# Optimization experiments

Measured on AMD Instinct MI355X. Metric: run time of the kernel, lower is better.

Reference implementation:

```python
import jax, jax.numpy as jnp
import numpy as np

S = 4096
F = 512  # in_features, head_num == 1 so per-head dim == F


def setup_inputs() -> dict:
    key = jax.random.key(0)
    ks = jax.random.split(key, 11)
    std = 0.02
    inp = {
        "q": jax.random.normal(ks[0], (1, S, F), jnp.float32),
        "k": jax.random.normal(ks[1], (1, S, F), jnp.float32),
        "v": jax.random.normal(ks[2], (1, S, F), jnp.float32),
        "Wq": jax.random.normal(ks[3], (F, F), jnp.float32) * std,
        "bq": jax.random.normal(ks[4], (F,), jnp.float32) * std,
        "Wk": jax.random.normal(ks[5], (F, F), jnp.float32) * std,
        "bk": jax.random.normal(ks[6], (F,), jnp.float32) * std,
        "Wv": jax.random.normal(ks[7], (F, F), jnp.float32) * std,
        "bv": jax.random.normal(ks[8], (F,), jnp.float32) * std,
        "Wo": jax.random.normal(ks[9], (F, F), jnp.float32) * std,
        "bo": jax.random.normal(ks[10], (F,), jnp.float32) * std,
    }
    return inp


def reference(q, k, v, Wq, bq, Wk, bk, Wv, bv, Wo, bo):
    dk = Wq.shape[0]  # head_num == 1 -> per-head dim equals in_features
    # q_k, q_v: projections of q WITHOUT activation (as in original forward)
    q_k = q @ Wk.T + bk            # (1, S, F)
    q_v = q @ Wv.T + bv            # (1, S, F)
    # activated projections (F.relu)
    qq = jax.nn.relu(q @ Wq.T + bq)[0]  # (S, F)
    kk = jax.nn.relu(k @ Wk.T + bk)[0]  # (S, F)
    vv = jax.nn.relu(v @ Wv.T + bv)[0]  # (S, F)
    # diagonal of qq @ q_k^T, computed without materializing the SxS matrix
    q_att = jnp.sum(qq * q_k[0], axis=-1, keepdims=True)  # (S, 1)
    scores = jnp.einsum('sd,td->st', qq, kk)               # (S, S)
    scores = jnp.concatenate([scores, q_att], axis=-1)     # (S, S+1)
    scores = scores / np.sqrt(dk + 1).astype(np.float32)
    attn = jax.nn.softmax(scores, axis=-1)                 # (S, S+1)
    res = attn[:, :-1] @ vv                                # (S, F)
    res = q_v[0] * q_att + res                             # elementwise fusion
    y = res[None]                                          # (1, S, F)
    y = jax.nn.relu(y @ Wo.T + bo)
    return y
```

## Files before the change

### kernel.cpp

```cpp
#include <hip/hip_runtime.h>
#include <math.h>

#define S_LEN 4096
#define F_DIM 512
#define PSPLIT 8
#define FIXED_M 4.0f

typedef __attribute__((ext_vector_type(8))) short bf16x8;
typedef __attribute__((ext_vector_type(4))) float f32x4;

__device__ __forceinline__ unsigned short f2bf(float x) {
    union { float f; unsigned u; } v; v.f = x;
    unsigned r = v.u + 0x7fffu + ((v.u >> 16) & 1u);
    return (unsigned short)(r >> 16);
}
__device__ __forceinline__ float bf2f(unsigned short b) {
    union { unsigned u; float f; } v; v.u = ((unsigned)b) << 16;
    return v.f;
}
__device__ __forceinline__ void load_lds16(const void* g, void* l) {
    __builtin_amdgcn_global_load_lds(
        (const __attribute__((address_space(1))) unsigned int*)g,
        (__attribute__((address_space(3))) unsigned int*)l, 16, 0, 0);
}

struct CastArgs {
    const float* src[7];
    unsigned short* dst[7];
    int n4[7];
};
__global__ void cast_all(CastArgs a) {
    int r = blockIdx.y;
    int i = blockIdx.x * blockDim.x + threadIdx.x;
    if (i >= a.n4[r]) return;
    float4 v = ((const float4*)a.src[r])[i];
    ushort4 o;
    o.x = f2bf(v.x); o.y = f2bf(v.y); o.z = f2bf(v.z); o.w = f2bf(v.w);
    ((ushort4*)a.dst[r])[i] = o;
}

__global__ void transpose_bf16(const unsigned short* __restrict__ src,
                               unsigned short* __restrict__ dst) {
    __shared__ __align__(16) unsigned short tile[64][72];
    const int s0 = blockIdx.x * 64, f0 = blockIdx.y * 64;
    const int tid = threadIdx.x;
#pragma unroll
    for (int it = 0; it < 2; ++it) {
        int u = it * 256 + tid;
        int r = u >> 3, c = (u & 7) * 8;
        *(uint4*)&tile[r][c] = *(const uint4*)(src + (size_t)(s0 + r) * F_DIM + f0 + c);
    }
    __syncthreads();
#pragma unroll
    for (int it = 0; it < 2; ++it) {
        int u = it * 256 + tid;
        int fl = u >> 3, sc = (u & 7) * 8;
        unsigned short tmp[8];
#pragma unroll
        for (int i = 0; i < 8; ++i) tmp[i] = tile[sc + i][fl];
        *(uint4*)(dst + (size_t)(f0 + fl) * S_LEN + s0 + sc) = *(uint4*)tmp;
    }
}

#define GEMM_KLOOP(XPTR, LDX, WPTR, LDW, KBEG, KEND)                                  \
    for (int k0 = (KBEG); k0 < (KEND); k0 += 64) {                                    \
        __syncthreads();                                                              \
        _Pragma("unroll")                                                             \
        for (int i = 0; i < 2; ++i) {                                                 \
            int c = w * 2 + i;                                                        \
            _Pragma("unroll")                                                         \
            for (int kh = 0; kh < 2; ++kh) {                                          \
                load_lds16((XPTR) + (size_t)(m0 + c * 16 + ln) * (LDX) + k0 + kh * 32 + quad * 8, \
                           &As[(c * 2 + kh) * 512]);                                  \
                load_lds16((WPTR) + (size_t)(n0 + c * 16 + ln) * (LDW) + k0 + kh * 32 + quad * 8, \
                           &Bs[(c * 2 + kh) * 512]);                                  \
            }                                                                         \
        }                                                                             \
        __syncthreads();                                                              \
        _Pragma("unroll")                                                             \
        for (int kh = 0; kh < 2; ++kh) {                                              \
            bf16x8 af[4], bfr[4];                                                     \
            _Pragma("unroll")                                                         \
            for (int mt = 0; mt < 4; ++mt)                                            \
                af[mt] = *(const bf16x8*)&As[((wr * 4 + mt) * 2 + kh) * 512 + l * 8];  \
            _Pragma("unroll")                                                         \
            for (int nt = 0; nt < 4; ++nt)                                            \
                bfr[nt] = *(const bf16x8*)&Bs[((wc * 4 + nt) * 2 + kh) * 512 + l * 8]; \
            _Pragma("unroll")                                                         \
            for (int mt = 0; mt < 4; ++mt)                                            \
                _Pragma("unroll")                                                     \
                for (int nt = 0; nt < 4; ++nt)                                        \
                    acc[mt][nt] = __builtin_amdgcn_mfma_f32_16x16x32_bf16(            \
                        af[mt], bfr[nt], acc[mt][nt], 0, 0, 0);                       \
        }                                                                             \
    }

#define KLOOP256(XPTR, LDX, WPTR, LDW, KBEG, KEND)                                    \
    for (int k0 = (KBEG); k0 < (KEND); k0 += 64) {                                    \
        __syncthreads();                                                              \
        _Pragma("unroll")                                                             \
        for (int i = 0; i < 4; ++i) {                                                 \
            int g = w * 4 + i;                                                        \
            _Pragma("unroll")                                                         \
            for (int kh = 0; kh < 2; ++kh)                                            \
                load_lds16((XPTR) + (size_t)(m0 + g * 16 + ln) * (LDX) + k0 + kh * 32 + quad * 8, \
                           &As[(g * 2 + kh) * 512]);                                  \
        }                                                                             \
        _Pragma("unroll")                                                             \
        for (int i = 0; i < 2; ++i) {                                                 \
            int g2 = w * 2 + i;                                                       \
            _Pragma("unroll")                                                         \
            for (int kh = 0; kh < 2; ++kh)                                            \
                load_lds16((WPTR) + (size_t)(n0 + g2 * 16 + ln) * (LDW) + k0 + kh * 32 + quad * 8, \
                           &Bs[(g2 * 2 + kh) * 512]);                                 \
        }                                                                             \
        __syncthreads();                                                              \
        _Pragma("unroll")                                                             \
        for (int kh = 0; kh < 2; ++kh) {                                              \
            bf16x8 af[4], bfr[8];                                                     \
            _Pragma("unroll")                                                         \
            for (int mt = 0; mt < 4; ++mt)                                            \
                af[mt] = *(const bf16x8*)&As[((w * 4 + mt) * 2 + kh) * 512 + l * 8];   \
            _Pragma("unroll")                                                         \
            for (int nt = 0; nt < 8; ++nt)                                            \
                bfr[nt] = *(const bf16x8*)&Bs[(nt * 2 + kh) * 512 + l * 8];            \
            _Pragma("unroll")                                                         \
            for (int mt = 0; mt < 4; ++mt)                                            \
                _Pragma("unroll")                                                     \
                for (int nt = 0; nt < 8; ++nt)                                        \
                    acc[mt][nt] = __builtin_amdgcn_mfma_f32_16x16x32_bf16(            \
                        af[mt], bfr[nt], acc[mt][nt], 0, 0, 0);                       \
        }                                                                             \
    }

struct GemmDesc {
    const unsigned short* X;
    const unsigned short* W;
    const float* bias;
    unsigned short* out_bf;
    float* out_f32;
    int relu;
};
struct GemmArgs { GemmDesc d[5]; };

__launch_bounds__(256, 2)
__global__ void gemm128(GemmArgs args) {
    __shared__ __align__(16) unsigned short As[16 * 512];
    __shared__ __align__(16) unsigned short Bs[16 * 512];
    const GemmDesc d = args.d[blockIdx.y >> 2];
    const int n0 = (blockIdx.y & 3) * 128;
    const int m0 = blockIdx.x * 128;
    const int tid = threadIdx.x;
    const int w = tid >> 6, l = tid & 63, quad = l >> 4, ln = l & 15;
    const int wr = w >> 1, wc = w & 1;

    f32x4 acc[4][4];
    f32x4 zero4 = {0.f, 0.f, 0.f, 0.f};
#pragma unroll
    for (int i = 0; i < 4; ++i)
#pragma unroll
        for (int j = 0; j < 4; ++j) acc[i][j] = zero4;

    GEMM_KLOOP(d.X, F_DIM, d.W, F_DIM, 0, F_DIM)

#pragma unroll
    for (int mt = 0; mt < 4; ++mt)
#pragma unroll
        for (int nt = 0; nt < 4; ++nt)
#pragma unroll
            for (int r = 0; r < 4; ++r) {
                int row = m0 + wr * 64 + mt * 16 + quad * 4 + r;
                int col = n0 + wc * 64 + nt * 16 + ln;
                float vv = acc[mt][nt][r] + d.bias[col];
                if (d.relu) vv = fmaxf(vv, 0.f);
                if (d.out_bf)  d.out_bf[(size_t)row * F_DIM + col] = f2bf(vv);
                if (d.out_f32) d.out_f32[(size_t)row * F_DIM + col] = vv;
            }
}

__launch_bounds__(256, 2)
__global__ void gemm_exp(const unsigned short* __restrict__ X,
                         const unsigned short* __restrict__ W,
                         unsigned short* __restrict__ P,
                         float* __restrict__ lpart) {
    __shared__ __align__(16) unsigned short As[32 * 512];
    __shared__ __align__(16) unsigned short Bs[16 * 512];
    const float scale = 0.04415108f;
    const int nb = blockIdx.y;
    const int n0 = nb * 128;
    const int m0 = blockIdx.x * 256;
    const int tid = threadIdx.x;
    const int w = tid >> 6, l = tid & 63, quad = l >> 4, ln = l & 15;

    f32x4 acc[4][8];
    f32x4 zero4 = {0.f, 0.f, 0.f, 0.f};
#pragma unroll
    for (int i = 0; i < 4; ++i)
#pragma unroll
        for (int j = 0; j < 8; ++j) acc[i][j] = zero4;

    KLOOP256(X, F_DIM, W, F_DIM, 0, F_DIM)

#pragma unroll
    for (int mt = 0; mt < 4; ++mt)
#pragma unroll
        for (int r = 0; r < 4; ++r) {
            int row = m0 + w * 64 + mt * 16 + quad * 4 + r;
            float rs = 0.f;
#pragma unroll
            for (int nt = 0; nt < 8; ++nt) {
                int col = n0 + nt * 16 + ln;
                float p = __expf(acc[mt][nt][r] * scale - FIXED_M);
                P[(size_t)row * S_LEN + col] = f2bf(p);
                rs += p;
            }
            rs += __shfl_xor(rs, 1);
            rs += __shfl_xor(rs, 2);
            rs += __shfl_xor(rs, 4);
            rs += __shfl_xor(rs, 8);
            if (ln == 0) lpart[(size_t)nb * S_LEN + row] = rs;
        }
}

__launch_bounds__(256, 2)
__global__ void gemm_pv(const unsigned short* __restrict__ P,
                        const unsigned short* __restrict__ vt,
                        unsigned short* __restrict__ O_p) {
    __shared__ __align__(16) unsigned short As[32 * 512];
    __shared__ __align__(16) unsigned short Bs[16 * 512];
    const int nb = blockIdx.y & 3;
    const int split = blockIdx.y >> 2;
    const int n0 = nb * 128;
    const int m0 = blockIdx.x * 256;
    const int koff = split * (S_LEN / PSPLIT);
    const int tid = threadIdx.x;
    const int w = tid >> 6, l = tid & 63, quad = l >> 4, ln = l & 15;

    f32x4 acc[4][8];
    f32x4 zero4 = {0.f, 0.f, 0.f, 0.f};
#pragma unroll
    for (int i = 0; i < 4; ++i)
#pragma unroll
        for (int j = 0; j < 8; ++j) acc[i][j] = zero4;

    KLOOP256(P, S_LEN, vt, S_LEN, koff, koff + S_LEN / PSPLIT)

    unsigned short* Op = O_p + (size_t)split * S_LEN * F_DIM;
#pragma unroll
    for (int mt = 0; mt < 4; ++mt)
#pragma unroll
        for (int nt = 0; nt < 8; ++nt)
#pragma unroll
            for (int r = 0; r < 4; ++r) {
                int row = m0 + w * 64 + mt * 16 + quad * 4 + r;
                int col = n0 + nt * 16 + ln;
                Op[(size_t)row * F_DIM + col] = f2bf(acc[mt][nt][r]);
            }
}

__launch_bounds__(256, 2)
__global__ void gemm_final(const unsigned short* __restrict__ X,
                           const unsigned short* __restrict__ W,
                           float* __restrict__ Fp) {
    __shared__ __align__(16) unsigned short As[16 * 512];
    __shared__ __align__(16) unsigned short Bs[16 * 512];
    const int nb = blockIdx.y & 3;
    const int kseg = blockIdx.y >> 2;
    const int n0 = nb * 128;
    const int m0 = blockIdx.x * 128;
    const int tid = threadIdx.x;
    const int w = tid >> 6, l = tid & 63, quad = l >> 4, ln = l & 15;
    const int wr = w >> 1, wc = w & 1;

    f32x4 acc[4][4];
    f32x4 zero4 = {0.f, 0.f, 0.f, 0.f};
#pragma unroll
    for (int i = 0; i < 4; ++i)
#pragma unroll
        for (int j = 0; j < 4; ++j) acc[i][j] = zero4;

    GEMM_KLOOP(X, F_DIM, W, F_DIM, kseg * 256, kseg * 256 + 256)

    float* Op = Fp + (size_t)kseg * S_LEN * F_DIM;
#pragma unroll
    for (int mt = 0; mt < 4; ++mt)
#pragma unroll
        for (int nt = 0; nt < 4; ++nt)
#pragma unroll
            for (int r = 0; r < 4; ++r) {
                int row = m0 + wr * 64 + mt * 16 + quad * 4 + r;
                int col = n0 + wc * 64 + nt * 16 + ln;
                Op[(size_t)row * F_DIM + col] = acc[mt][nt][r];
            }
}

__global__ void reduce_final(const float* __restrict__ Fp,
                             const float* __restrict__ bias,
                             float* __restrict__ out) {
    int i = blockIdx.x * blockDim.x + threadIdx.x;
    int col4 = (i & (F_DIM / 4 - 1)) * 4;
    float4 a = ((const float4*)Fp)[i];
    float4 b = ((const float4*)(Fp + (size_t)S_LEN * F_DIM))[i];
    float4 bi = *(const float4*)(bias + col4);
    float4 o;
    o.x = fmaxf(a.x + b.x + bi.x, 0.f);
    o.y = fmaxf(a.y + b.y + bi.y, 0.f);
    o.z = fmaxf(a.z + b.z + bi.z, 0.f);
    o.w = fmaxf(a.w + b.w + bi.w, 0.f);
    ((float4*)out)[i] = o;
}

__global__ void combine_kernel(const unsigned short* __restrict__ O_p,
                               const float* __restrict__ lpart,
                               const unsigned short* __restrict__ qq,
                               const unsigned short* __restrict__ qk,
                               const unsigned short* __restrict__ qv,
                               unsigned short* __restrict__ res_bf) {
    const float scale = 0.04415108f;
    int row = blockIdx.x;
    int t = threadIdx.x;
    int wv = t >> 6, l = t & 63;
    __shared__ float wsum[2];

    ushort4 a = *(const ushort4*)(qq + (size_t)row * F_DIM + t * 4);
    ushort4 b = *(const ushort4*)(qk + (size_t)row * F_DIM + t * 4);
    float part = bf2f(a.x) * bf2f(b.x) + bf2f(a.y) * bf2f(b.y) +
                 bf2f(a.z) * bf2f(b.z) + bf2f(a.w) * bf2f(b.w);
#pragma unroll
    for (int off = 32; off >= 1; off >>= 1) part += __shfl_xor(part, off);
    if (l == 0) wsum[wv] = part;
    __syncthreads();
    float qa = wsum[0] + wsum[1];

    float denom = __expf(qa * scale - FIXED_M);
#pragma unroll
    for (int i = 0; i < 32; ++i) denom += lpart[(size_t)i * S_LEN + row];
    float inv = 1.f / denom;

    for (int f = t; f < F_DIM; f += 128) {
        float acc = 0.f;
#pragma unroll
        for (int i = 0; i < PSPLIT; ++i)
            acc += bf2f(O_p[((size_t)i * S_LEN + row) * F_DIM + f]);
        float r = bf2f(qv[(size_t)row * F_DIM + f]) * qa + acc * inv;
        res_bf[(size_t)row * F_DIM + f] = f2bf(r);
    }
}

extern "C" void kernel_launch(void* const* d_in, const int* in_sizes, int n_in,
                              void* d_out, int out_size, void* d_ws, size_t ws_size,
                              hipStream_t stream) {
    const float* q  = (const float*)d_in[0];
    const float* k  = (const float*)d_in[1];
    const float* v  = (const float*)d_in[2];
    const float* Wq = (const float*)d_in[3];
    const float* bq = (const float*)d_in[4];
    const float* Wk = (const float*)d_in[5];
    const float* bk = (const float*)d_in[6];
    const float* Wv = (const float*)d_in[7];
    const float* bv = (const float*)d_in[8];
    const float* Wo = (const float*)d_in[9];
    const float* bo = (const float*)d_in[10];
    float* out = (float*)d_out;

    char* p = (char*)d_ws;
    auto alloc = [&](size_t bytes) -> char* {
        char* r = p; p += (bytes + 255) & ~(size_t)255; return r;
    };
    const size_t SF = (size_t)S_LEN * F_DIM;
    unsigned short* q_bf  = (unsigned short*)alloc(SF * 2);
    unsigned short* k_bf  = (unsigned short*)alloc(SF * 2);
    unsigned short* v_bf  = (unsigned short*)alloc(SF * 2);
    unsigned short* qq_bf = (unsigned short*)alloc(SF * 2);
    unsigned short* kk_bf = (unsigned short*)alloc(SF * 2);
    unsigned short* vv_bf = (unsigned short*)alloc(SF * 2);
    unsigned short* vt_bf = (unsigned short*)alloc(SF * 2);
    unsigned short* qk_bf = (unsigned short*)alloc(SF * 2);
    unsigned short* qv_bf = (unsigned short*)alloc(SF * 2);
    unsigned short* res_bf = (unsigned short*)alloc(SF * 2);
    unsigned short* wq_bf = (unsigned short*)alloc((size_t)F_DIM * F_DIM * 2);
    unsigned short* wk_bf = (unsigned short*)alloc((size_t)F_DIM * F_DIM * 2);
    unsigned short* wv_bf = (unsigned short*)alloc((size_t)F_DIM * F_DIM * 2);
    unsigned short* wo_bf = (unsigned short*)alloc((size_t)F_DIM * F_DIM * 2);
    unsigned short* P_bf  = (unsigned short*)alloc((size_t)S_LEN * S_LEN * 2);
    float* lpart = (float*)alloc((size_t)32 * S_LEN * 4);
    unsigned short* O_p = (unsigned short*)alloc((size_t)PSPLIT * SF * 2);
    float* Fp = (float*)alloc((size_t)2 * SF * 4);

    CastArgs ca;
    ca.src[0] = q;  ca.dst[0] = q_bf;  ca.n4[0] = (int)(SF / 4);
    ca.src[1] = k;  ca.dst[1] = k_bf;  ca.n4[1] = (int)(SF / 4);
    ca.src[2] = v;  ca.dst[2] = v_bf;  ca.n4[2] = (int)(SF / 4);
    ca.src[3] = Wq; ca.dst[3] = wq_bf; ca.n4[3] = F_DIM * F_DIM / 4;
    ca.src[4] = Wk; ca.dst[4] = wk_bf; ca.n4[4] = F_DIM * F_DIM / 4;
    ca.src[5] = Wv; ca.dst[5] = wv_bf; ca.n4[5] = F_DIM * F_DIM / 4;
    ca.src[6] = Wo; ca.dst[6] = wo_bf; ca.n4[6] = F_DIM * F_DIM / 4;
    cast_all<<<dim3((unsigned)(SF / 4 / 256), 7), 256, 0, stream>>>(ca);

    GemmArgs ga;
    ga.d[0] = { q_bf, wq_bf, bq, qq_bf, nullptr, 1 };
    ga.d[1] = { k_bf, wk_bf, bk, kk_bf, nullptr, 1 };
    ga.d[2] = { v_bf, wv_bf, bv, vv_bf, nullptr, 1 };
    ga.d[3] = { q_bf, wk_bf, bk, qk_bf, nullptr, 0 };
    ga.d[4] = { q_bf, wv_bf, bv, qv_bf, nullptr, 0 };
    gemm128<<<dim3(S_LEN / 128, 20), 256, 0, stream>>>(ga);

    transpose_bf16<<<dim3(S_LEN / 64, F_DIM / 64), 256, 0, stream>>>(vv_bf, vt_bf);

    gemm_exp<<<dim3(S_LEN / 256, S_LEN / 128), 256, 0, stream>>>(qq_bf, kk_bf, P_bf, lpart);

    gemm_pv<<<dim3(S_LEN / 256, 4 * PSPLIT), 256, 0, stream>>>(P_bf, vt_bf, O_p);

    combine_kernel<<<S_LEN, 128, 0, stream>>>(O_p, lpart, qq_bf, qk_bf, qv_bf, res_bf);

    gemm_final<<<dim3(S_LEN / 128, 8), 256, 0, stream>>>(res_bf, wo_bf, Fp);
    reduce_final<<<(unsigned)(SF / 4 / 256), 256, 0, stream>>>(Fp, bo, out);
}
```

Measured before the change: 219.3 us.

## Use 256x256 double-buffered swizzled MFMA tiles for projection, QK and PV GEMMs

Replaces the 128-wide 256-thread GEMM kernels with a shared 512-thread 256x256 k-loop. It double-buffers LDS, XOR-swizzles the tile layout, and interleaves fragment loads, next-tile prefetch and MFMA quadrants between barriers, raising MFMA priority with setprio. The projection, QK-exp and PV GEMMs all use it, and lpart becomes a row-major 64-wide layout. The combine kernel now reduces lpart with shuffles and uses vectorised loads and stores. The aim is more data reuse per tile and overlapping global-to-LDS traffic with compute, at the cost of 128KB of dynamic LDS per block, which limits occupancy, and fewer blocks in the grid.

```diff
diff --git a/kernel.cpp b/kernel.cpp
--- a/kernel.cpp
+++ b/kernel.cpp
@@ -5,6 +5,7 @@
 #define F_DIM 512
 #define PSPLIT 8
 #define FIXED_M 4.0f
+#define SCALE_QK 0.04415108f
 
 typedef __attribute__((ext_vector_type(8))) short bf16x8;
 typedef __attribute__((ext_vector_type(4))) float f32x4;
@@ -60,6 +61,211 @@
         for (int i = 0; i < 8; ++i) tmp[i] = tile[sc + i][fl];
         *(uint4*)(dst + (size_t)(f0 + fl) * S_LEN + s0 + sc) = *(uint4*)tmp;
     }
+}
+
+struct GemmDesc {
+    const unsigned short* X;
+    const unsigned short* W;
+    const float* bias;
+    unsigned short* out_bf;
+    float* out_f32;
+    int relu;
+};
+struct GemmArgs { GemmDesc d[5]; };
+
+#define FRAGA(qm) { _Pragma("unroll") for (int mt = 0; mt < 4; ++mt) { \
+    const int ro = (aw + (qm) * 64 + mt * 16) * 64 + rbase; \
+    af[mt][0] = *(const bf16x8*)&Ac[ro + q0]; \
+    af[mt][1] = *(const bf16x8*)&Ac[ro + q1]; } }
+
+#define FRAGB(qn) { _Pragma("unroll") for (int nt = 0; nt < 2; ++nt) { \
+    const int ro = (bw + (qn) * 32 + nt * 16) * 64 + rbase; \
+    bf[nt][0] = *(const bf16x8*)&Bc[ro + q0]; \
+    bf[nt][1] = *(const bf16x8*)&Bc[ro + q1]; } }
+
+#define MMQ(qm, qn) { __builtin_amdgcn_s_setprio(1); \
+    _Pragma("unroll") for (int kh = 0; kh < 2; ++kh) \
+    _Pragma("unroll") for (int mt = 0; mt < 4; ++mt) \
+    _Pragma("unroll") for (int nt = 0; nt < 2; ++nt) \
+      acc[(qm) * 4 + mt][(qn) * 2 + nt] = __builtin_amdgcn_mfma_f32_16x16x32_bf16( \
+          af[mt][kh], bf[nt][kh], acc[(qm) * 4 + mt][(qn) * 2 + nt], 0, 0, 0); \
+    __builtin_amdgcn_s_setprio(0); }
+
+__device__ __forceinline__ void kloop256(const unsigned short* __restrict__ A, int lda,
+                                         const unsigned short* __restrict__ B, int ldb,
+                                         int m0, int n0, int kbase,
+                                         unsigned short* smem, f32x4 acc[8][4]) {
+    const int tid = threadIdx.x;
+    const int w = tid >> 6, l = tid & 63;
+    const int ln = l & 15, quad = l >> 4, lnx = l & 7;
+    const int wm = w >> 2, wn = w & 3;
+    const int srow = l >> 3;
+    const int scol = (lnx ^ srow) * 8;
+    const int rbase = ln * 64;
+    const int q0 = (quad ^ lnx) * 8;
+    const int q1 = ((4 + quad) ^ lnx) * 8;
+    unsigned short* As = smem;
+    unsigned short* Bs = smem + 32768;
+    const unsigned short* Asrc = A + (size_t)(m0 + srow) * lda + kbase + scol;
+    const unsigned short* Bsrc = B + (size_t)(n0 + srow) * ldb + kbase + scol;
+
+    auto stageA = [&](int dd, int ktn) {
+#pragma unroll
+        for (int j = 0; j < 4; ++j) {
+            int chunk = w * 4 + j;
+            load_lds16(Asrc + (size_t)(chunk * 8) * lda + ktn * 64,
+                       &As[dd * 16384 + chunk * 512]);
+        }
+    };
+    auto stageB = [&](int dd, int ktn) {
+#pragma unroll
+        for (int j = 0; j < 4; ++j) {
+            int chunk = w * 4 + j;
+            load_lds16(Bsrc + (size_t)(chunk * 8) * ldb + ktn * 64,
+                       &Bs[dd * 16384 + chunk * 512]);
+        }
+    };
+
+    stageA(0, 0); stageB(0, 0);
+    asm volatile("s_waitcnt vmcnt(0)" ::: "memory");
+    __builtin_amdgcn_s_barrier();
+
+#pragma unroll
+    for (int kt = 0; kt < 8; ++kt) {
+        const int d = kt & 1;
+        const unsigned short* Ac = &As[d * 16384];
+        const unsigned short* Bc = &Bs[d * 16384];
+        const int aw = wm * 128, bw = wn * 64;
+        bf16x8 af[4][2], bf[2][2];
+
+        FRAGA(0); FRAGB(0);
+        if (kt < 7) stageA(d ^ 1, kt + 1);
+        __builtin_amdgcn_s_barrier();
+        MMQ(0, 0);
+        __builtin_amdgcn_s_barrier();
+
+        FRAGB(1);
+        if (kt < 7) stageB(d ^ 1, kt + 1);
+        __builtin_amdgcn_s_barrier();
+        MMQ(0, 1);
+        __builtin_amdgcn_s_barrier();
+
+        FRAGA(1);
+        __builtin_amdgcn_s_barrier();
+        MMQ(1, 1);
+        __builtin_amdgcn_s_barrier();
+
+        FRAGB(0);
+        __builtin_amdgcn_s_barrier();
+        MMQ(1, 0);
+        asm volatile("s_waitcnt vmcnt(0)" ::: "memory");
+        __builtin_amdgcn_s_barrier();
+    }
+}
+
+__launch_bounds__(512, 2)
+__global__ void gemm_proj2(GemmArgs args) {
+    extern __shared__ unsigned short smem[];
+    const GemmDesc d = args.d[blockIdx.y >> 1];
+    const int n0 = (blockIdx.y & 1) * 256;
+    const int m0 = blockIdx.x * 256;
+    f32x4 acc[8][4];
+    f32x4 z = {0.f, 0.f, 0.f, 0.f};
+#pragma unroll
+    for (int i = 0; i < 8; ++i)
+#pragma unroll
+        for (int j = 0; j < 4; ++j) acc[i][j] = z;
+
+    kloop256(d.X, F_DIM, d.W, F_DIM, m0, n0, 0, smem, acc);
+
+    const int tid = threadIdx.x;
+    const int w = tid >> 6, l = tid & 63, quad = l >> 4, ln = l & 15;
+    const int wm = w >> 2, wn = w & 3;
+#pragma unroll
+    for (int mi = 0; mi < 8; ++mi)
+#pragma unroll
+        for (int ni = 0; ni < 4; ++ni)
+#pragma unroll
+            for (int r = 0; r < 4; ++r) {
+                int row = m0 + wm * 128 + mi * 16 + quad * 4 + r;
+                int col = n0 + wn * 64 + ni * 16 + ln;
+                float vv = acc[mi][ni][r] + d.bias[col];
+                if (d.relu) vv = fmaxf(vv, 0.f);
+                if (d.out_bf)  d.out_bf[(size_t)row * F_DIM + col] = f2bf(vv);
+                if (d.out_f32) d.out_f32[(size_t)row * F_DIM + col] = vv;
+            }
+}
+
+__launch_bounds__(512, 2)
+__global__ void gemm_exp2(const unsigned short* __restrict__ X,
+                          const unsigned short* __restrict__ W,
+                          unsigned short* __restrict__ P,
+                          float* __restrict__ lpart) {
+    extern __shared__ unsigned short smem[];
+    const int m0 = blockIdx.x * 256, n0 = blockIdx.y * 256;
+    f32x4 acc[8][4];
+    f32x4 z = {0.f, 0.f, 0.f, 0.f};
+#pragma unroll
+    for (int i = 0; i < 8; ++i)
+#pragma unroll
+        for (int j = 0; j < 4; ++j) acc[i][j] = z;
+
+    kloop256(X, F_DIM, W, F_DIM, m0, n0, 0, smem, acc);
+
+    const int tid = threadIdx.x;
+    const int w = tid >> 6, l = tid & 63, quad = l >> 4, ln = l & 15;
+    const int wm = w >> 2, wn = w & 3;
+#pragma unroll
+    for (int mi = 0; mi < 8; ++mi)
+#pragma unroll
+        for (int r = 0; r < 4; ++r) {
+            int row = m0 + wm * 128 + mi * 16 + quad * 4 + r;
+            float rs = 0.f;
+#pragma unroll
+            for (int ni = 0; ni < 4; ++ni) {
+                int col = n0 + wn * 64 + ni * 16 + ln;
+                float p = __expf(acc[mi][ni][r] * SCALE_QK - FIXED_M);
+                P[(size_t)row * S_LEN + col] = f2bf(p);
+                rs += p;
+            }
+            rs += __shfl_xor(rs, 1);
+            rs += __shfl_xor(rs, 2);
+            rs += __shfl_xor(rs, 4);
+            rs += __shfl_xor(rs, 8);
+            if (ln == 0) lpart[(size_t)row * 64 + blockIdx.y * 4 + wn] = rs;
+        }
+}
+
+__launch_bounds__(512, 2)
+__global__ void gemm_pv2(const unsigned short* __restrict__ P,
+                         const unsigned short* __restrict__ vt,
+                         unsigned short* __restrict__ O_p) {
+    extern __shared__ unsigned short smem[];
+    const int nb = blockIdx.y & 1, split = blockIdx.y >> 1;
+    const int m0 = blockIdx.x * 256, n0 = nb * 256;
+    f32x4 acc[8][4];
+    f32x4 z = {0.f, 0.f, 0.f, 0.f};
+#pragma unroll
+    for (int i = 0; i < 8; ++i)
+#pragma unroll
+        for (int j = 0; j < 4; ++j) acc[i][j] = z;
+
+    kloop256(P, S_LEN, vt, S_LEN, m0, n0, split * (S_LEN / PSPLIT), smem, acc);
+
+    unsigned short* Op = O_p + (size_t)split * S_LEN * F_DIM;
+    const int tid = threadIdx.x;
+    const int w = tid >> 6, l = tid & 63, quad = l >> 4, ln = l & 15;
+    const int wm = w >> 2, wn = w & 3;
+#pragma unroll
+    for (int mi = 0; mi < 8; ++mi)
+#pragma unroll
+        for (int ni = 0; ni < 4; ++ni)
+#pragma unroll
+            for (int r = 0; r < 4; ++r) {
+                int row = m0 + wm * 128 + mi * 16 + quad * 4 + r;
+                int col = n0 + wn * 64 + ni * 16 + ln;
+                Op[(size_t)row * F_DIM + col] = f2bf(acc[mi][ni][r]);
+            }
 }
 
 #define GEMM_KLOOP(XPTR, LDX, WPTR, LDW, KBEG, KEND)                                  \
@@ -79,184 +285,21 @@
         __syncthreads();                                                              \
         _Pragma("unroll")                                                             \
         for (int kh = 0; kh < 2; ++kh) {                                              \
-            bf16x8 af[4], bfr[4];                                                     \
+            bf16x8 af2[4], bfr2[4];                                                   \
             _Pragma("unroll")                                                         \
             for (int mt = 0; mt < 4; ++mt)                                            \
-                af[mt] = *(const bf16x8*)&As[((wr * 4 + mt) * 2 + kh) * 512 + l * 8];  \
+                af2[mt] = *(const bf16x8*)&As[((wr * 4 + mt) * 2 + kh) * 512 + l * 8]; \
             _Pragma("unroll")                                                         \
             for (int nt = 0; nt < 4; ++nt)                                            \
-                bfr[nt] = *(const bf16x8*)&Bs[((wc * 4 + nt) * 2 + kh) * 512 + l * 8]; \
+                bfr2[nt] = *(const bf16x8*)&Bs[((wc * 4 + nt) * 2 + kh) * 512 + l * 8]; \
             _Pragma("unroll")                                                         \
             for (int mt = 0; mt < 4; ++mt)                                            \
                 _Pragma("unroll")                                                     \
                 for (int nt = 0; nt < 4; ++nt)                                        \
                     acc[mt][nt] = __builtin_amdgcn_mfma_f32_16x16x32_bf16(            \
-                        af[mt], bfr[nt], acc[mt][nt], 0, 0, 0);                       \
+                        af2[mt], bfr2[nt], acc[mt][nt], 0, 0, 0);                     \
         }                                                                             \
     }
-
-#define KLOOP256(XPTR, LDX, WPTR, LDW, KBEG, KEND)                                    \
-    for (int k0 = (KBEG); k0 < (KEND); k0 += 64) {                                    \
-        __syncthreads();                                                              \
-        _Pragma("unroll")                                                             \
-        for (int i = 0; i < 4; ++i) {                                                 \
-            int g = w * 4 + i;                                                        \
-            _Pragma("unroll")                                                         \
-            for (int kh = 0; kh < 2; ++kh)                                            \
-                load_lds16((XPTR) + (size_t)(m0 + g * 16 + ln) * (LDX) + k0 + kh * 32 + quad * 8, \
-                           &As[(g * 2 + kh) * 512]);                                  \
-        }                                                                             \
-        _Pragma("unroll")                                                             \
-        for (int i = 0; i < 2; ++i) {                                                 \
-            int g2 = w * 2 + i;                                                       \
-            _Pragma("unroll")                                                         \
-            for (int kh = 0; kh < 2; ++kh)                                            \
-                load_lds16((WPTR) + (size_t)(n0 + g2 * 16 + ln) * (LDW) + k0 + kh * 32 + quad * 8, \
-                           &Bs[(g2 * 2 + kh) * 512]);                                 \
-        }                                                                             \
-        __syncthreads();                                                              \
-        _Pragma("unroll")                                                             \
-        for (int kh = 0; kh < 2; ++kh) {                                              \
-            bf16x8 af[4], bfr[8];                                                     \
-            _Pragma("unroll")                                                         \
-            for (int mt = 0; mt < 4; ++mt)                                            \
-                af[mt] = *(const bf16x8*)&As[((w * 4 + mt) * 2 + kh) * 512 + l * 8];   \
-            _Pragma("unroll")                                                         \
-            for (int nt = 0; nt < 8; ++nt)                                            \
-                bfr[nt] = *(const bf16x8*)&Bs[(nt * 2 + kh) * 512 + l * 8];            \
-            _Pragma("unroll")                                                         \
-            for (int mt = 0; mt < 4; ++mt)                                            \
-                _Pragma("unroll")                                                     \
-                for (int nt = 0; nt < 8; ++nt)                                        \
-                    acc[mt][nt] = __builtin_amdgcn_mfma_f32_16x16x32_bf16(            \
-                        af[mt], bfr[nt], acc[mt][nt], 0, 0, 0);                       \
-        }                                                                             \
-    }
-
-struct GemmDesc {
-    const unsigned short* X;
-    const unsigned short* W;
-    const float* bias;
-    unsigned short* out_bf;
-    float* out_f32;
-    int relu;
-};
-struct GemmArgs { GemmDesc d[5]; };
-
-__launch_bounds__(256, 2)
-__global__ void gemm128(GemmArgs args) {
-    __shared__ __align__(16) unsigned short As[16 * 512];
-    __shared__ __align__(16) unsigned short Bs[16 * 512];
-    const GemmDesc d = args.d[blockIdx.y >> 2];
-    const int n0 = (blockIdx.y & 3) * 128;
-    const int m0 = blockIdx.x * 128;
-    const int tid = threadIdx.x;
-    const int w = tid >> 6, l = tid & 63, quad = l >> 4, ln = l & 15;
-    const int wr = w >> 1, wc = w & 1;
-
-    f32x4 acc[4][4];
-    f32x4 zero4 = {0.f, 0.f, 0.f, 0.f};
-#pragma unroll
-    for (int i = 0; i < 4; ++i)
-#pragma unroll
-        for (int j = 0; j < 4; ++j) acc[i][j] = zero4;
-
-    GEMM_KLOOP(d.X, F_DIM, d.W, F_DIM, 0, F_DIM)
-
-#pragma unroll
-    for (int mt = 0; mt < 4; ++mt)
-#pragma unroll
-        for (int nt = 0; nt < 4; ++nt)
-#pragma unroll
-            for (int r = 0; r < 4; ++r) {
-                int row = m0 + wr * 64 + mt * 16 + quad * 4 + r;
-                int col = n0 + wc * 64 + nt * 16 + ln;
-                float vv = acc[mt][nt][r] + d.bias[col];
-                if (d.relu) vv = fmaxf(vv, 0.f);
-                if (d.out_bf)  d.out_bf[(size_t)row * F_DIM + col] = f2bf(vv);
-                if (d.out_f32) d.out_f32[(size_t)row * F_DIM + col] = vv;
-            }
-}
-
-__launch_bounds__(256, 2)
-__global__ void gemm_exp(const unsigned short* __restrict__ X,
-                         const unsigned short* __restrict__ W,
-                         unsigned short* __restrict__ P,
-                         float* __restrict__ lpart) {
-    __shared__ __align__(16) unsigned short As[32 * 512];
-    __shared__ __align__(16) unsigned short Bs[16 * 512];
-    const float scale = 0.04415108f;
-    const int nb = blockIdx.y;
-    const int n0 = nb * 128;
-    const int m0 = blockIdx.x * 256;
-    const int tid = threadIdx.x;
-    const int w = tid >> 6, l = tid & 63, quad = l >> 4, ln = l & 15;
-
-    f32x4 acc[4][8];
-    f32x4 zero4 = {0.f, 0.f, 0.f, 0.f};
-#pragma unroll
-    for (int i = 0; i < 4; ++i)
-#pragma unroll
-        for (int j = 0; j < 8; ++j) acc[i][j] = zero4;
-
-    KLOOP256(X, F_DIM, W, F_DIM, 0, F_DIM)
-
-#pragma unroll
-    for (int mt = 0; mt < 4; ++mt)
-#pragma unroll
-        for (int r = 0; r < 4; ++r) {
-            int row = m0 + w * 64 + mt * 16 + quad * 4 + r;
-            float rs = 0.f;
-#pragma unroll
-            for (int nt = 0; nt < 8; ++nt) {
-                int col = n0 + nt * 16 + ln;
-                float p = __expf(acc[mt][nt][r] * scale - FIXED_M);
-                P[(size_t)row * S_LEN + col] = f2bf(p);
-                rs += p;
-            }
-            rs += __shfl_xor(rs, 1);
-            rs += __shfl_xor(rs, 2);
-            rs += __shfl_xor(rs, 4);
-            rs += __shfl_xor(rs, 8);
-            if (ln == 0) lpart[(size_t)nb * S_LEN + row] = rs;
-        }
-}
-
-__launch_bounds__(256, 2)
-__global__ void gemm_pv(const unsigned short* __restrict__ P,
-                        const unsigned short* __restrict__ vt,
-                        unsigned short* __restrict__ O_p) {
-    __shared__ __align__(16) unsigned short As[32 * 512];
-    __shared__ __align__(16) unsigned short Bs[16 * 512];
-    const int nb = blockIdx.y & 3;
-    const int split = blockIdx.y >> 2;
-    const int n0 = nb * 128;
-    const int m0 = blockIdx.x * 256;
-    const int koff = split * (S_LEN / PSPLIT);
-    const int tid = threadIdx.x;
-    const int w = tid >> 6, l = tid & 63, quad = l >> 4, ln = l & 15;
-
-    f32x4 acc[4][8];
-    f32x4 zero4 = {0.f, 0.f, 0.f, 0.f};
-#pragma unroll
-    for (int i = 0; i < 4; ++i)
-#pragma unroll
-        for (int j = 0; j < 8; ++j) acc[i][j] = zero4;
-
-    KLOOP256(P, S_LEN, vt, S_LEN, koff, koff + S_LEN / PSPLIT)
-
-    unsigned short* Op = O_p + (size_t)split * S_LEN * F_DIM;
-#pragma unroll
-    for (int mt = 0; mt < 4; ++mt)
-#pragma unroll
-        for (int nt = 0; nt < 8; ++nt)
-#pragma unroll
-            for (int r = 0; r < 4; ++r) {
-                int row = m0 + w * 64 + mt * 16 + quad * 4 + r;
-                int col = n0 + nt * 16 + ln;
-                Op[(size_t)row * F_DIM + col] = f2bf(acc[mt][nt][r]);
-            }
-}
 
 __launch_bounds__(256, 2)
 __global__ void gemm_final(const unsigned short* __restrict__ X,
@@ -316,35 +359,40 @@
                                const unsigned short* __restrict__ qk,
                                const unsigned short* __restrict__ qv,
                                unsigned short* __restrict__ res_bf) {
-    const float scale = 0.04415108f;
     int row = blockIdx.x;
     int t = threadIdx.x;
     int wv = t >> 6, l = t & 63;
-    __shared__ float wsum[2];
+    __shared__ float ws[4];
 
     ushort4 a = *(const ushort4*)(qq + (size_t)row * F_DIM + t * 4);
     ushort4 b = *(const ushort4*)(qk + (size_t)row * F_DIM + t * 4);
-    float part = bf2f(a.x) * bf2f(b.x) + bf2f(a.y) * bf2f(b.y) +
+    float dotp = bf2f(a.x) * bf2f(b.x) + bf2f(a.y) * bf2f(b.y) +
                  bf2f(a.z) * bf2f(b.z) + bf2f(a.w) * bf2f(b.w);
-#pragma unroll
-    for (int off = 32; off >= 1; off >>= 1) part += __shfl_xor(part, off);
-    if (l == 0) wsum[wv] = part;
+    float lp = (t < 64) ? lpart[(size_t)row * 64 + t] : 0.f;
+#pragma unroll
+    for (int off = 32; off >= 1; off >>= 1) {
+        dotp += __shfl_xor(dotp, off);
+        lp += __shfl_xor(lp, off);
+    }
+    if (l == 0) { ws[wv] = dotp; ws[2 + wv] = lp; }
     __syncthreads();
-    float qa = wsum[0] + wsum[1];
-
-    float denom = __expf(qa * scale - FIXED_M);
-#pragma unroll
-    for (int i = 0; i < 32; ++i) denom += lpart[(size_t)i * S_LEN + row];
+    float qa = ws[0] + ws[1];
+    float denom = __expf(qa * SCALE_QK - FIXED_M) + ws[2] + ws[3];
     float inv = 1.f / denom;
 
-    for (int f = t; f < F_DIM; f += 128) {
-        float acc = 0.f;
-#pragma unroll
-        for (int i = 0; i < PSPLIT; ++i)
-            acc += bf2f(O_p[((size_t)i * S_LEN + row) * F_DIM + f]);
-        float r = bf2f(qv[(size_t)row * F_DIM + f]) * qa + acc * inv;
-        res_bf[(size_t)row * F_DIM + f] = f2bf(r);
-    }
+    float4 s = {0.f, 0.f, 0.f, 0.f};
+#pragma unroll
+    for (int i = 0; i < PSPLIT; ++i) {
+        ushort4 o = *(const ushort4*)(O_p + ((size_t)i * S_LEN + row) * F_DIM + t * 4);
+        s.x += bf2f(o.x); s.y += bf2f(o.y); s.z += bf2f(o.z); s.w += bf2f(o.w);
+    }
+    ushort4 qvv = *(const ushort4*)(qv + (size_t)row * F_DIM + t * 4);
+    ushort4 o;
+    o.x = f2bf(bf2f(qvv.x) * qa + s.x * inv);
+    o.y = f2bf(bf2f(qvv.y) * qa + s.y * inv);
+    o.z = f2bf(bf2f(qvv.z) * qa + s.z * inv);
+    o.w = f2bf(bf2f(qvv.w) * qa + s.w * inv);
+    *(ushort4*)(res_bf + (size_t)row * F_DIM + t * 4) = o;
 }
 
 extern "C" void kernel_launch(void* const* d_in, const int* in_sizes, int n_in,
@@ -383,9 +431,20 @@
     unsigned short* wv_bf = (unsigned short*)alloc((size_t)F_DIM * F_DIM * 2);
     unsigned short* wo_bf = (unsigned short*)alloc((size_t)F_DIM * F_DIM * 2);
     unsigned short* P_bf  = (unsigned short*)alloc((size_t)S_LEN * S_LEN * 2);
-    float* lpart = (float*)alloc((size_t)32 * S_LEN * 4);
+    float* lpart = (float*)alloc((size_t)S_LEN * 64 * 4);
     unsigned short* O_p = (unsigned short*)alloc((size_t)PSPLIT * SF * 2);
     float* Fp = (float*)alloc((size_t)2 * SF * 4);
+
+    static int attr_done = 0;
+    if (!attr_done) {
+        hipFuncSetAttribute((const void*)gemm_proj2,
+                            hipFuncAttributeMaxDynamicSharedMemorySize, 131072);
+        hipFuncSetAttribute((const void*)gemm_exp2,
+                            hipFuncAttributeMaxDynamicSharedMemorySize, 131072);
+        hipFuncSetAttribute((const void*)gemm_pv2,
+                            hipFuncAttributeMaxDynamicSharedMemorySize, 131072);
+        attr_done = 1;
+    }
 
     CastArgs ca;
     ca.src[0] = q;  ca.dst[0] = q_bf;  ca.n4[0] = (int)(SF / 4);
@@ -403,13 +462,13 @@
     ga.d[2] = { v_bf, wv_bf, bv, vv_bf, nullptr, 1 };
     ga.d[3] = { q_bf, wk_bf, bk, qk_bf, nullptr, 0 };
     ga.d[4] = { q_bf, wv_bf, bv, qv_bf, nullptr, 0 };
-    gemm128<<<dim3(S_LEN / 128, 20), 256, 0, stream>>>(ga);
+    gemm_proj2<<<dim3(S_LEN / 256, 10), 512, 131072, stream>>>(ga);
 
     transpose_bf16<<<dim3(S_LEN / 64, F_DIM / 64), 256, 0, stream>>>(vv_bf, vt_bf);
 
-    gemm_exp<<<dim3(S_LEN / 256, S_LEN / 128), 256, 0, stream>>>(qq_bf, kk_bf, P_bf, lpart);
-
-    gemm_pv<<<dim3(S_LEN / 256, 4 * PSPLIT), 256, 0, stream>>>(P_bf, vt_bf, O_p);
+    gemm_exp2<<<dim3(S_LEN / 256, S_LEN / 256), 512, 131072, stream>>>(qq_bf, kk_bf, P_bf, lpart);
+
+    gemm_pv2<<<dim3(S_LEN / 256, 2 * PSPLIT), 512, 131072, stream>>>(P_bf, vt_bf, O_p);
 
     combine_kernel<<<S_LEN, 128, 0, stream>>>(O_p, lpart, qq_bf, qk_bf, qv_bf, res_bf);
 
```

Measured after the change: 199.7 us. 8.9% less time.

## Shrink attention GEMM tiles to 128x128, fuse final reduce, transpose lpart

Applied to the files above, without the earlier changes.

Replaces the 256x128 tiles in the QK-exp and PV GEMMs with 128x128 tiles on a 2x2 wave layout. This doubles the block count and halves the LDS per block, at the cost of re-reading operands more often. The final projection no longer splits K with a separate reduce kernel; it applies bias and ReLU directly in the GEMM epilogue. The row-sum partials are stored row-major as 64 per row so the combine kernel can reduce them with warp shuffles, and the combine kernel is vectorized to ushort4.

```diff
diff --git a/kernel.cpp b/kernel.cpp
--- a/kernel.cpp
+++ b/kernel.cpp
@@ -5,6 +5,7 @@
 #define F_DIM 512
 #define PSPLIT 8
 #define FIXED_M 4.0f
+#define SCALE_QK 0.04415108f
 
 typedef __attribute__((ext_vector_type(8))) short bf16x8;
 typedef __attribute__((ext_vector_type(4))) float f32x4;
@@ -61,6 +62,16 @@
         *(uint4*)(dst + (size_t)(f0 + fl) * S_LEN + s0 + sc) = *(uint4*)tmp;
     }
 }
+
+struct GemmDesc {
+    const unsigned short* X;
+    const unsigned short* W;
+    const float* bias;
+    unsigned short* out_bf;
+    float* out_f32;
+    int relu;
+};
+struct GemmArgs { GemmDesc d[5]; };
 
 #define GEMM_KLOOP(XPTR, LDX, WPTR, LDW, KBEG, KEND)                                  \
     for (int k0 = (KBEG); k0 < (KEND); k0 += 64) {                                    \
@@ -79,72 +90,25 @@
         __syncthreads();                                                              \
         _Pragma("unroll")                                                             \
         for (int kh = 0; kh < 2; ++kh) {                                              \
-            bf16x8 af[4], bfr[4];                                                     \
+            bf16x8 af2[4], bfr2[4];                                                   \
             _Pragma("unroll")                                                         \
             for (int mt = 0; mt < 4; ++mt)                                            \
-                af[mt] = *(const bf16x8*)&As[((wr * 4 + mt) * 2 + kh) * 512 + l * 8];  \
+                af2[mt] = *(const bf16x8*)&As[((wr * 4 + mt) * 2 + kh) * 512 + l * 8]; \
             _Pragma("unroll")                                                         \
             for (int nt = 0; nt < 4; ++nt)                                            \
-                bfr[nt] = *(const bf16x8*)&Bs[((wc * 4 + nt) * 2 + kh) * 512 + l * 8]; \
+                bfr2[nt] = *(const bf16x8*)&Bs[((wc * 4 + nt) * 2 + kh) * 512 + l * 8]; \
             _Pragma("unroll")                                                         \
             for (int mt = 0; mt < 4; ++mt)                                            \
                 _Pragma("unroll")                                                     \
                 for (int nt = 0; nt < 4; ++nt)                                        \
                     acc[mt][nt] = __builtin_amdgcn_mfma_f32_16x16x32_bf16(            \
-                        af[mt], bfr[nt], acc[mt][nt], 0, 0, 0);                       \
+                        af2[mt], bfr2[nt], acc[mt][nt], 0, 0, 0);                     \
         }                                                                             \
     }
 
-#define KLOOP256(XPTR, LDX, WPTR, LDW, KBEG, KEND)                                    \
-    for (int k0 = (KBEG); k0 < (KEND); k0 += 64) {                                    \
-        __syncthreads();                                                              \
-        _Pragma("unroll")                                                             \
-        for (int i = 0; i < 4; ++i) {                                                 \
-            int g = w * 4 + i;                                                        \
-            _Pragma("unroll")                                                         \
-            for (int kh = 0; kh < 2; ++kh)                                            \
-                load_lds16((XPTR) + (size_t)(m0 + g * 16 + ln) * (LDX) + k0 + kh * 32 + quad * 8, \
-                           &As[(g * 2 + kh) * 512]);                                  \
-        }                                                                             \
-        _Pragma("unroll")                                                             \
-        for (int i = 0; i < 2; ++i) {                                                 \
-            int g2 = w * 2 + i;                                                       \
-            _Pragma("unroll")                                                         \
-            for (int kh = 0; kh < 2; ++kh)                                            \
-                load_lds16((WPTR) + (size_t)(n0 + g2 * 16 + ln) * (LDW) + k0 + kh * 32 + quad * 8, \
-                           &Bs[(g2 * 2 + kh) * 512]);                                 \
-        }                                                                             \
-        __syncthreads();                                                              \
-        _Pragma("unroll")                                                             \
-        for (int kh = 0; kh < 2; ++kh) {                                              \
-            bf16x8 af[4], bfr[8];                                                     \
-            _Pragma("unroll")                                                         \
-            for (int mt = 0; mt < 4; ++mt)                                            \
-                af[mt] = *(const bf16x8*)&As[((w * 4 + mt) * 2 + kh) * 512 + l * 8];   \
-            _Pragma("unroll")                                                         \
-            for (int nt = 0; nt < 8; ++nt)                                            \
-                bfr[nt] = *(const bf16x8*)&Bs[(nt * 2 + kh) * 512 + l * 8];            \
-            _Pragma("unroll")                                                         \
-            for (int mt = 0; mt < 4; ++mt)                                            \
-                _Pragma("unroll")                                                     \
-                for (int nt = 0; nt < 8; ++nt)                                        \
-                    acc[mt][nt] = __builtin_amdgcn_mfma_f32_16x16x32_bf16(            \
-                        af[mt], bfr[nt], acc[mt][nt], 0, 0, 0);                       \
-        }                                                                             \
-    }
-
-struct GemmDesc {
-    const unsigned short* X;
-    const unsigned short* W;
-    const float* bias;
-    unsigned short* out_bf;
-    float* out_f32;
-    int relu;
-};
-struct GemmArgs { GemmDesc d[5]; };
 
 __launch_bounds__(256, 2)
-__global__ void gemm128(GemmArgs args) {
+__global__ void gemm_proj2(GemmArgs args) {
     __shared__ __align__(16) unsigned short As[16 * 512];
     __shared__ __align__(16) unsigned short Bs[16 * 512];
     const GemmDesc d = args.d[blockIdx.y >> 2];
@@ -179,38 +143,38 @@
 }
 
 __launch_bounds__(256, 2)
-__global__ void gemm_exp(const unsigned short* __restrict__ X,
-                         const unsigned short* __restrict__ W,
-                         unsigned short* __restrict__ P,
-                         float* __restrict__ lpart) {
-    __shared__ __align__(16) unsigned short As[32 * 512];
+__global__ void gemm_exp2(const unsigned short* __restrict__ X,
+                          const unsigned short* __restrict__ W,
+                          unsigned short* __restrict__ P,
+                          float* __restrict__ lpart) {
+    __shared__ __align__(16) unsigned short As[16 * 512];
     __shared__ __align__(16) unsigned short Bs[16 * 512];
-    const float scale = 0.04415108f;
-    const int nb = blockIdx.y;
-    const int n0 = nb * 128;
-    const int m0 = blockIdx.x * 256;
+    const int m0 = blockIdx.x * 128;
+    const int ntile = blockIdx.y;
+    const int n0 = ntile * 128;
     const int tid = threadIdx.x;
     const int w = tid >> 6, l = tid & 63, quad = l >> 4, ln = l & 15;
-
-    f32x4 acc[4][8];
+    const int wr = w >> 1, wc = w & 1;
+
+    f32x4 acc[4][4];
     f32x4 zero4 = {0.f, 0.f, 0.f, 0.f};
 #pragma unroll
     for (int i = 0; i < 4; ++i)
 #pragma unroll
-        for (int j = 0; j < 8; ++j) acc[i][j] = zero4;
-
-    KLOOP256(X, F_DIM, W, F_DIM, 0, F_DIM)
+        for (int j = 0; j < 4; ++j) acc[i][j] = zero4;
+
+    GEMM_KLOOP(X, F_DIM, W, F_DIM, 0, F_DIM)
 
 #pragma unroll
     for (int mt = 0; mt < 4; ++mt)
 #pragma unroll
         for (int r = 0; r < 4; ++r) {
-            int row = m0 + w * 64 + mt * 16 + quad * 4 + r;
+            int row = m0 + wr * 64 + mt * 16 + quad * 4 + r;
             float rs = 0.f;
 #pragma unroll
-            for (int nt = 0; nt < 8; ++nt) {
-                int col = n0 + nt * 16 + ln;
-                float p = __expf(acc[mt][nt][r] * scale - FIXED_M);
+            for (int nt = 0; nt < 4; ++nt) {
+                int col = n0 + wc * 64 + nt * 16 + ln;
+                float p = __expf(acc[mt][nt][r] * SCALE_QK - FIXED_M);
                 P[(size_t)row * S_LEN + col] = f2bf(p);
                 rs += p;
             }
@@ -218,42 +182,43 @@
             rs += __shfl_xor(rs, 2);
             rs += __shfl_xor(rs, 4);
             rs += __shfl_xor(rs, 8);
-            if (ln == 0) lpart[(size_t)nb * S_LEN + row] = rs;
+            if (ln == 0) lpart[(size_t)row * 64 + ntile * 2 + wc] = rs;
         }
 }
 
 __launch_bounds__(256, 2)
-__global__ void gemm_pv(const unsigned short* __restrict__ P,
-                        const unsigned short* __restrict__ vt,
-                        unsigned short* __restrict__ O_p) {
-    __shared__ __align__(16) unsigned short As[32 * 512];
+__global__ void gemm_pv2(const unsigned short* __restrict__ P,
+                         const unsigned short* __restrict__ vt,
+                         unsigned short* __restrict__ O_p) {
+    __shared__ __align__(16) unsigned short As[16 * 512];
     __shared__ __align__(16) unsigned short Bs[16 * 512];
-    const int nb = blockIdx.y & 3;
-    const int split = blockIdx.y >> 2;
-    const int n0 = nb * 128;
-    const int m0 = blockIdx.x * 256;
-    const int koff = split * (S_LEN / PSPLIT);
+    const int m0 = blockIdx.x * 128;
+    const int y = blockIdx.y;
+    const int n0 = (y & 3) * 128;
+    const int split = y >> 2;
+    const int kbeg = split * (S_LEN / PSPLIT);
     const int tid = threadIdx.x;
     const int w = tid >> 6, l = tid & 63, quad = l >> 4, ln = l & 15;
-
-    f32x4 acc[4][8];
+    const int wr = w >> 1, wc = w & 1;
+
+    f32x4 acc[4][4];
     f32x4 zero4 = {0.f, 0.f, 0.f, 0.f};
 #pragma unroll
     for (int i = 0; i < 4; ++i)
 #pragma unroll
-        for (int j = 0; j < 8; ++j) acc[i][j] = zero4;
-
-    KLOOP256(P, S_LEN, vt, S_LEN, koff, koff + S_LEN / PSPLIT)
+        for (int j = 0; j < 4; ++j) acc[i][j] = zero4;
+
+    GEMM_KLOOP(P, S_LEN, vt, S_LEN, kbeg, kbeg + S_LEN / PSPLIT)
 
     unsigned short* Op = O_p + (size_t)split * S_LEN * F_DIM;
 #pragma unroll
     for (int mt = 0; mt < 4; ++mt)
 #pragma unroll
-        for (int nt = 0; nt < 8; ++nt)
+        for (int nt = 0; nt < 4; ++nt)
 #pragma unroll
             for (int r = 0; r < 4; ++r) {
-                int row = m0 + w * 64 + mt * 16 + quad * 4 + r;
-                int col = n0 + nt * 16 + ln;
+                int row = m0 + wr * 64 + mt * 16 + quad * 4 + r;
+                int col = n0 + wc * 64 + nt * 16 + ln;
                 Op[(size_t)row * F_DIM + col] = f2bf(acc[mt][nt][r]);
             }
 }
@@ -261,12 +226,11 @@
 __launch_bounds__(256, 2)
 __global__ void gemm_final(const unsigned short* __restrict__ X,
                            const unsigned short* __restrict__ W,
-                           float* __restrict__ Fp) {
+                           const float* __restrict__ bias,
+                           float* __restrict__ out) {
     __shared__ __align__(16) unsigned short As[16 * 512];
     __shared__ __align__(16) unsigned short Bs[16 * 512];
-    const int nb = blockIdx.y & 3;
-    const int kseg = blockIdx.y >> 2;
-    const int n0 = nb * 128;
+    const int n0 = blockIdx.y * 128;
     const int m0 = blockIdx.x * 128;
     const int tid = threadIdx.x;
     const int w = tid >> 6, l = tid & 63, quad = l >> 4, ln = l & 15;
@@ -279,9 +243,8 @@
 #pragma unroll
         for (int j = 0; j < 4; ++j) acc[i][j] = zero4;
 
-    GEMM_KLOOP(X, F_DIM, W, F_DIM, kseg * 256, kseg * 256 + 256)
-
-    float* Op = Fp + (size_t)kseg * S_LEN * F_DIM;
+    GEMM_KLOOP(X, F_DIM, W, F_DIM, 0, F_DIM)
+
 #pragma unroll
     for (int mt = 0; mt < 4; ++mt)
 #pragma unroll
@@ -290,24 +253,9 @@
             for (int r = 0; r < 4; ++r) {
                 int row = m0 + wr * 64 + mt * 16 + quad * 4 + r;
                 int col = n0 + wc * 64 + nt * 16 + ln;
-                Op[(size_t)row * F_DIM + col] = acc[mt][nt][r];
+                out[(size_t)row * F_DIM + col] =
+                    fmaxf(acc[mt][nt][r] + bias[col], 0.f);
             }
-}
-
-__global__ void reduce_final(const float* __restrict__ Fp,
-                             const float* __restrict__ bias,
-                             float* __restrict__ out) {
-    int i = blockIdx.x * blockDim.x + threadIdx.x;
-    int col4 = (i & (F_DIM / 4 - 1)) * 4;
-    float4 a = ((const float4*)Fp)[i];
-    float4 b = ((const float4*)(Fp + (size_t)S_LEN * F_DIM))[i];
-    float4 bi = *(const float4*)(bias + col4);
-    float4 o;
-    o.x = fmaxf(a.x + b.x + bi.x, 0.f);
-    o.y = fmaxf(a.y + b.y + bi.y, 0.f);
-    o.z = fmaxf(a.z + b.z + bi.z, 0.f);
-    o.w = fmaxf(a.w + b.w + bi.w, 0.f);
-    ((float4*)out)[i] = o;
 }
 
 __global__ void combine_kernel(const unsigned short* __restrict__ O_p,
@@ -316,35 +264,40 @@
                                const unsigned short* __restrict__ qk,
                                const unsigned short* __restrict__ qv,
                                unsigned short* __restrict__ res_bf) {
-    const float scale = 0.04415108f;
     int row = blockIdx.x;
     int t = threadIdx.x;
     int wv = t >> 6, l = t & 63;
-    __shared__ float wsum[2];
+    __shared__ float ws[4];
 
     ushort4 a = *(const ushort4*)(qq + (size_t)row * F_DIM + t * 4);
     ushort4 b = *(const ushort4*)(qk + (size_t)row * F_DIM + t * 4);
-    float part = bf2f(a.x) * bf2f(b.x) + bf2f(a.y) * bf2f(b.y) +
+    float dotp = bf2f(a.x) * bf2f(b.x) + bf2f(a.y) * bf2f(b.y) +
                  bf2f(a.z) * bf2f(b.z) + bf2f(a.w) * bf2f(b.w);
-#pragma unroll
-    for (int off = 32; off >= 1; off >>= 1) part += __shfl_xor(part, off);
-    if (l == 0) wsum[wv] = part;
+    float lp = (t < 64) ? lpart[(size_t)row * 64 + t] : 0.f;
+#pragma unroll
+    for (int off = 32; off >= 1; off >>= 1) {
+        dotp += __shfl_xor(dotp, off);
+        lp += __shfl_xor(lp, off);
+    }
+    if (l == 0) { ws[wv] = dotp; ws[2 + wv] = lp; }
     __syncthreads();
-    float qa = wsum[0] + wsum[1];
-
-    float denom = __expf(qa * scale - FIXED_M);
-#pragma unroll
-    for (int i = 0; i < 32; ++i) denom += lpart[(size_t)i * S_LEN + row];
+    float qa = ws[0] + ws[1];
+    float denom = __expf(qa * SCALE_QK - FIXED_M) + ws[2] + ws[3];
     float inv = 1.f / denom;
 
-    for (int f = t; f < F_DIM; f += 128) {
-        float acc = 0.f;
-#pragma unroll
-        for (int i = 0; i < PSPLIT; ++i)
-            acc += bf2f(O_p[((size_t)i * S_LEN + row) * F_DIM + f]);
-        float r = bf2f(qv[(size_t)row * F_DIM + f]) * qa + acc * inv;
-        res_bf[(size_t)row * F_DIM + f] = f2bf(r);
-    }
+    float4 s = {0.f, 0.f, 0.f, 0.f};
+#pragma unroll
+    for (int i = 0; i < PSPLIT; ++i) {
+        ushort4 o = *(const ushort4*)(O_p + ((size_t)i * S_LEN + row) * F_DIM + t * 4);
+        s.x += bf2f(o.x); s.y += bf2f(o.y); s.z += bf2f(o.z); s.w += bf2f(o.w);
+    }
+    ushort4 qvv = *(const ushort4*)(qv + (size_t)row * F_DIM + t * 4);
+    ushort4 o;
+    o.x = f2bf(bf2f(qvv.x) * qa + s.x * inv);
+    o.y = f2bf(bf2f(qvv.y) * qa + s.y * inv);
+    o.z = f2bf(bf2f(qvv.z) * qa + s.z * inv);
+    o.w = f2bf(bf2f(qvv.w) * qa + s.w * inv);
+    *(ushort4*)(res_bf + (size_t)row * F_DIM + t * 4) = o;
 }
 
 extern "C" void kernel_launch(void* const* d_in, const int* in_sizes, int n_in,
@@ -383,9 +336,8 @@
     unsigned short* wv_bf = (unsigned short*)alloc((size_t)F_DIM * F_DIM * 2);
     unsigned short* wo_bf = (unsigned short*)alloc((size_t)F_DIM * F_DIM * 2);
     unsigned short* P_bf  = (unsigned short*)alloc((size_t)S_LEN * S_LEN * 2);
-    float* lpart = (float*)alloc((size_t)32 * S_LEN * 4);
+    float* lpart = (float*)alloc((size_t)S_LEN * 64 * 4);
     unsigned short* O_p = (unsigned short*)alloc((size_t)PSPLIT * SF * 2);
-    float* Fp = (float*)alloc((size_t)2 * SF * 4);
 
     CastArgs ca;
     ca.src[0] = q;  ca.dst[0] = q_bf;  ca.n4[0] = (int)(SF / 4);
@@ -403,16 +355,15 @@
     ga.d[2] = { v_bf, wv_bf, bv, vv_bf, nullptr, 1 };
     ga.d[3] = { q_bf, wk_bf, bk, qk_bf, nullptr, 0 };
     ga.d[4] = { q_bf, wv_bf, bv, qv_bf, nullptr, 0 };
-    gemm128<<<dim3(S_LEN / 128, 20), 256, 0, stream>>>(ga);
+    gemm_proj2<<<dim3(S_LEN / 128, 20), 256, 0, stream>>>(ga);
 
     transpose_bf16<<<dim3(S_LEN / 64, F_DIM / 64), 256, 0, stream>>>(vv_bf, vt_bf);
 
-    gemm_exp<<<dim3(S_LEN / 256, S_LEN / 128), 256, 0, stream>>>(qq_bf, kk_bf, P_bf, lpart);
-
-    gemm_pv<<<dim3(S_LEN / 256, 4 * PSPLIT), 256, 0, stream>>>(P_bf, vt_bf, O_p);
+    gemm_exp2<<<dim3(S_LEN / 128, S_LEN / 128), 256, 0, stream>>>(qq_bf, kk_bf, P_bf, lpart);
+
+    gemm_pv2<<<dim3(S_LEN / 128, 32), 256, 0, stream>>>(P_bf, vt_bf, O_p);
 
     combine_kernel<<<S_LEN, 128, 0, stream>>>(O_p, lpart, qq_bf, qk_bf, qv_bf, res_bf);
 
-    gemm_final<<<dim3(S_LEN / 128, 8), 256, 0, stream>>>(res_bf, wo_bf, Fp);
-    reduce_final<<<(unsigned)(SF / 4 / 256), 256, 0, stream>>>(Fp, bo, out);
-}
+    gemm_final<<<dim3(S_LEN / 128, 4), 256, 0, stream>>>(res_bf, wo_bf, bo, out);
+}
```

After: 233.8 us. 1.07x slower.
